# Kernel optimization log

Hardware: AMD Instinct MI355X
Metric: run time of the kernel (lower is better)

Reference implementation:

```python
import jax, jax.numpy as jnp
import numpy as np

B, N, D, L = 4, 512, 128, 2


def setup_inputs() -> dict:
    key = jax.random.key(0)
    ks = jax.random.split(key, 6)
    node_feats = jax.random.normal(ks[0], (B, N, D), dtype=jnp.float32)
    adj_mask = jax.random.uniform(ks[1], (B, N, N), dtype=jnp.float32)
    # torch Linear weights: [out_features, in_features]
    w1 = jax.random.normal(ks[2], (L, D, 2 * D), dtype=jnp.float32) * 0.05
    b1 = jax.random.normal(ks[3], (L, D), dtype=jnp.float32) * 0.05
    w2 = jax.random.normal(ks[4], (L, D, D), dtype=jnp.float32) * 0.05
    b2 = jax.random.normal(ks[5], (L, D), dtype=jnp.float32) * 0.05
    return {"node_feats": node_feats, "adj_mask": adj_mask,
            "w1": w1, "b1": b1, "w2": w2, "b2": b2}


def reference(node_feats, adj_mask, w1, b1, w2, b2):
    h = node_feats
    d = h.shape[-1]
    n_layers = w1.shape[0]
    for l in range(n_layers):
        # cat([hi, hj]) @ W1^T == hi @ Wi^T + hj @ Wj^T  (avoid 2D concat)
        wi = w1[l][:, :d]   # [D, D]
        wj = w1[l][:, d:]   # [D, D]
        ai = jnp.einsum('bnd,od->bno', h, wi)  # contribution of node i
        aj = jnp.einsum('bnd,od->bno', h, wj)  # contribution of node j
        # [B, N(i), N(j), D]
        m = jax.nn.relu(ai[:, :, None, :] + aj[:, None, :, :] + b1[l])
        m = jnp.einsum('bijd,od->bijo', m, w2[l]) + b2[l]
        m = m * adj_mask[..., None]
        msg = m.sum(axis=2)  # sum over j
        h = h + msg
    return h
```

## Files before the change

kernel.cpp:

```cpp
#include <hip/hip_runtime.h>


constexpr int Bc = 4, Nc = 512, Dc = 128, Lc = 2;
constexpr int BN = Bc * Nc;
constexpr int TIB = 4;
constexpr int TN = 4;

__global__ void transpose_w_kernel(const float* __restrict__ w1,
                                   const float* __restrict__ w2,
                                   float* __restrict__ wiT,
                                   float* __restrict__ wjT,
                                   float* __restrict__ w2T) {
    int idx = blockIdx.x * blockDim.x + threadIdx.x;
    if (idx >= Lc * Dc * Dc) return;
    int l = idx / (Dc * Dc);
    int rem = idx - l * Dc * Dc;
    int d = rem / Dc;
    int o = rem - d * Dc;
    wiT[idx] = w1[(l * Dc + o) * (2 * Dc) + d];
    wjT[idx] = w1[(l * Dc + o) * (2 * Dc) + Dc + d];
    w2T[idx] = w2[(l * Dc + o) * Dc + d];
}

__global__ __launch_bounds__(128) void gnn_lin1(const float* __restrict__ h,
                                                const float* __restrict__ wiT,
                                                const float* __restrict__ wjT,
                                                const float* __restrict__ b1,
                                                float* __restrict__ ai,
                                                float* __restrict__ aj) {
    __shared__ float hs[TN][Dc];
    const int o = threadIdx.x;
    const int r0 = blockIdx.x * TN;
#pragma unroll
    for (int t = 0; t < TN; ++t) hs[t][o] = h[(size_t)(r0 + t) * Dc + o];
    __syncthreads();
    float acci[TN], accj[TN];
    const float bo = b1[o];
#pragma unroll
    for (int t = 0; t < TN; ++t) { acci[t] = bo; accj[t] = 0.f; }
    for (int d = 0; d < Dc; d += 4) {
        float wi[4], wj[4];
#pragma unroll
        for (int k = 0; k < 4; ++k) {
            wi[k] = wiT[(size_t)(d + k) * Dc + o];
            wj[k] = wjT[(size_t)(d + k) * Dc + o];
        }
#pragma unroll
        for (int t = 0; t < TN; ++t) {
            const float4 hv = *reinterpret_cast<const float4*>(&hs[t][d]);
            acci[t] = fmaf(hv.x, wi[0], acci[t]);
            acci[t] = fmaf(hv.y, wi[1], acci[t]);
            acci[t] = fmaf(hv.z, wi[2], acci[t]);
            acci[t] = fmaf(hv.w, wi[3], acci[t]);
            accj[t] = fmaf(hv.x, wj[0], accj[t]);
            accj[t] = fmaf(hv.y, wj[1], accj[t]);
            accj[t] = fmaf(hv.z, wj[2], accj[t]);
            accj[t] = fmaf(hv.w, wj[3], accj[t]);
        }
    }
#pragma unroll
    for (int t = 0; t < TN; ++t) {
        ai[(size_t)(r0 + t) * Dc + o] = acci[t];
        aj[(size_t)(r0 + t) * Dc + o] = accj[t];
    }
}

template <bool HAS_NEXT>
__global__ __launch_bounds__(512) void gnn_msgfull(
    const float* __restrict__ ai, const float* __restrict__ aj,
    const float* __restrict__ adj, const float* __restrict__ hin,
    const float* __restrict__ w2T, const float* __restrict__ b2,
    const float* __restrict__ wiT, const float* __restrict__ wjT,
    const float* __restrict__ b1, float* __restrict__ hout,
    float* __restrict__ ai_out, float* __restrict__ aj_out) {
    __shared__ __align__(16) float adjs[TIB][Nc];
    __shared__ __align__(16) float scratch[4096];
    __shared__ float s_lds[TIB][Dc];
    __shared__ float hnew_lds[TIB][Dc];
    __shared__ float redw[8];

    const int tid = threadIdx.x;
    const int w = tid >> 6;
    const int lane = tid & 63;
    const int r0 = blockIdx.x * TIB;
    const int b = r0 >> 9;
    const int i0 = r0 & (Nc - 1);
    const float* __restrict__ ajb = aj + (size_t)b * Nc * Dc;
    const float* __restrict__ adjb = adj + (size_t)b * Nc * Nc;

    {
        const int rr = tid >> 7;
        const int c4 = (tid & 127) * 4;
        const float4 av =
            *reinterpret_cast<const float4*>(&adjb[(size_t)(i0 + rr) * Nc + c4]);
        *reinterpret_cast<float4*>(&adjs[rr][c4]) = av;
        float p = av.x + av.y + av.z + av.w;
#pragma unroll
        for (int m = 32; m >= 1; m >>= 1) p += __shfl_xor(p, m);
        if (lane == 0) redw[w] = p;
    }

    const int jlane = lane >> 5;
    const int dq = (lane & 31) * 4;
    float4 x[TIB], acc[TIB];
#pragma unroll
    for (int r = 0; r < TIB; ++r) {
        x[r] = *reinterpret_cast<const float4*>(&ai[(size_t)(r0 + r) * Dc + dq]);
        acc[r] = make_float4(0.f, 0.f, 0.f, 0.f);
    }
    __syncthreads();

    const int jw = w * 64;
    const float* __restrict__ pbase = ajb + (size_t)(jw + jlane) * Dc + dq;
#pragma unroll 4
    for (int it = 0; it < 32; ++it) {
        const float4 v = *reinterpret_cast<const float4*>(pbase + (size_t)it * 256);
        const int j = jw + 2 * it + jlane;
        const float a0 = adjs[0][j];
        const float a1 = adjs[1][j];
        const float a2 = adjs[2][j];
        const float a3 = adjs[3][j];
#define ROWF(r, a)                                                       \
        acc[r].x = fmaf(a, fmaxf(x[r].x + v.x, 0.f), acc[r].x);          \
        acc[r].y = fmaf(a, fmaxf(x[r].y + v.y, 0.f), acc[r].y);          \
        acc[r].z = fmaf(a, fmaxf(x[r].z + v.z, 0.f), acc[r].z);          \
        acc[r].w = fmaf(a, fmaxf(x[r].w + v.w, 0.f), acc[r].w);
        ROWF(0, a0) ROWF(1, a1) ROWF(2, a2) ROWF(3, a3)
#undef ROWF
    }

#pragma unroll
    for (int r = 0; r < TIB; ++r) {
        acc[r].x += __shfl_xor(acc[r].x, 32);
        acc[r].y += __shfl_xor(acc[r].y, 32);
        acc[r].z += __shfl_xor(acc[r].z, 32);
        acc[r].w += __shfl_xor(acc[r].w, 32);
    }
    if (lane < 32) {
#pragma unroll
        for (int r = 0; r < TIB; ++r)
            *reinterpret_cast<float4*>(&scratch[w * 512 + r * 128 + dq]) = acc[r];
    }
    __syncthreads();

    {
        const int rr = tid >> 7;
        const int dd = tid & 127;
        float s = 0.f;
#pragma unroll
        for (int ww = 0; ww < 8; ++ww) s += scratch[ww * 512 + rr * 128 + dd];
        s_lds[rr][dd] = s;
    }
    __syncthreads();

    {
        const int o = tid & 127;
        const int g = tid >> 7;
        float part[TIB] = {0.f, 0.f, 0.f, 0.f};
        for (int dd = g * 32; dd < g * 32 + 32; dd += 4) {
            float wv[4];
#pragma unroll
            for (int k = 0; k < 4; ++k) wv[k] = w2T[(size_t)(dd + k) * Dc + o];
#pragma unroll
            for (int r = 0; r < TIB; ++r) {
                const float4 sv = *reinterpret_cast<const float4*>(&s_lds[r][dd]);
                part[r] = fmaf(sv.x, wv[0], part[r]);
                part[r] = fmaf(sv.y, wv[1], part[r]);
                part[r] = fmaf(sv.z, wv[2], part[r]);
                part[r] = fmaf(sv.w, wv[3], part[r]);
            }
        }
#pragma unroll
        for (int r = 0; r < TIB; ++r) scratch[g * 512 + r * 128 + o] = part[r];
    }
    __syncthreads();

    {
        const int rr = tid >> 7;
        const int o = tid & 127;
        float a2c = scratch[rr * 128 + o] + scratch[512 + rr * 128 + o] +
                    scratch[1024 + rr * 128 + o] + scratch[1536 + rr * 128 + o];
        const float arow_r = redw[2 * rr] + redw[2 * rr + 1];
        const float hn =
            hin[(size_t)(r0 + rr) * Dc + o] + a2c + arow_r * b2[o];
        hout[(size_t)(r0 + rr) * Dc + o] = hn;
        if constexpr (HAS_NEXT) hnew_lds[rr][o] = hn;
    }

    if constexpr (HAS_NEXT) {
        __syncthreads();
        {
            const int o = tid & 127;
            const int g = tid >> 7;
            float pi[TIB] = {0.f, 0.f, 0.f, 0.f};
            float pj[TIB] = {0.f, 0.f, 0.f, 0.f};
            for (int dd = g * 32; dd < g * 32 + 32; dd += 4) {
                float wiv[4], wjv[4];
#pragma unroll
                for (int k = 0; k < 4; ++k) {
                    wiv[k] = wiT[(size_t)(dd + k) * Dc + o];
                    wjv[k] = wjT[(size_t)(dd + k) * Dc + o];
                }
#pragma unroll
                for (int r = 0; r < TIB; ++r) {
                    const float4 hv =
                        *reinterpret_cast<const float4*>(&hnew_lds[r][dd]);
                    pi[r] = fmaf(hv.x, wiv[0], pi[r]);
                    pi[r] = fmaf(hv.y, wiv[1], pi[r]);
                    pi[r] = fmaf(hv.z, wiv[2], pi[r]);
                    pi[r] = fmaf(hv.w, wiv[3], pi[r]);
                    pj[r] = fmaf(hv.x, wjv[0], pj[r]);
                    pj[r] = fmaf(hv.y, wjv[1], pj[r]);
                    pj[r] = fmaf(hv.z, wjv[2], pj[r]);
                    pj[r] = fmaf(hv.w, wjv[3], pj[r]);
                }
            }
#pragma unroll
            for (int r = 0; r < TIB; ++r) {
                scratch[g * 512 + r * 128 + o] = pi[r];
                scratch[2048 + g * 512 + r * 128 + o] = pj[r];
            }
        }
        __syncthreads();
        {
            const int rr = tid >> 7;
            const int o = tid & 127;
            float acci = b1[o];
            float accj = 0.f;
#pragma unroll
            for (int g = 0; g < 4; ++g) {
                acci += scratch[g * 512 + rr * 128 + o];
                accj += scratch[2048 + g * 512 + rr * 128 + o];
            }
            ai_out[(size_t)(r0 + rr) * Dc + o] = acci;
            aj_out[(size_t)(r0 + rr) * Dc + o] = accj;
        }
    }
}

extern "C" void kernel_launch(void* const* d_in, const int* in_sizes, int n_in,
                              void* d_out, int out_size, void* d_ws, size_t ws_size,
                              hipStream_t stream) {
    const float* node = (const float*)d_in[0];
    const float* adj  = (const float*)d_in[1];
    const float* w1   = (const float*)d_in[2];
    const float* b1   = (const float*)d_in[3];
    const float* w2   = (const float*)d_in[4];
    const float* b2   = (const float*)d_in[5];
    float* out = (float*)d_out;

    float* ws = (float*)d_ws;
    float* wiT = ws; ws += Lc * Dc * Dc;
    float* wjT = ws; ws += Lc * Dc * Dc;
    float* w2T = ws; ws += Lc * Dc * Dc;
    float* ai  = ws; ws += BN * Dc;
    float* aj  = ws; ws += BN * Dc;
    float* ai2 = ws; ws += BN * Dc;
    float* aj2 = ws; ws += BN * Dc;
    float* h1  = ws; ws += BN * Dc;

    transpose_w_kernel<<<(Lc * Dc * Dc + 255) / 256, 256, 0, stream>>>(
        w1, w2, wiT, wjT, w2T);

    gnn_lin1<<<BN / TN, 128, 0, stream>>>(node, wiT, wjT, b1, ai, aj);
    gnn_msgfull<true><<<BN / TIB, 512, 0, stream>>>(
        ai, aj, adj, node, w2T, b2, wiT + Dc * Dc, wjT + Dc * Dc, b1 + Dc,
        h1, ai2, aj2);
    gnn_msgfull<false><<<BN / TIB, 512, 0, stream>>>(
        ai2, aj2, adj, h1, w2T + Dc * Dc, b2 + Dc, nullptr, nullptr, nullptr,
        out, nullptr, nullptr);
}
```

Baseline: 55.02 us.

## Fuse all GNN stages into one cooperative kernel with grid syncs

Replaces the four separate launches (weight transpose, first linear, two message layers) with a single cooperative persistent kernel of 512 blocks x 256 threads that uses grid.sync between phases. Block size drops from 512 to 256 threads, and each thread covers more j and d work. The aim is to remove launch gaps and kernel-boundary overhead. The cost is grid-wide barrier latency and lower per-block parallelism, and it needs at least 2 resident blocks per CU, otherwise it falls back to the old path.

```diff
diff --git a/kernel.cpp b/kernel.cpp
--- a/kernel.cpp
+++ b/kernel.cpp
@@ -1,10 +1,239 @@
 #include <hip/hip_runtime.h>
+#include <hip/hip_cooperative_groups.h>
+
+namespace cg = cooperative_groups;
 
 
 constexpr int Bc = 4, Nc = 512, Dc = 128, Lc = 2;
 constexpr int BN = Bc * Nc;
 constexpr int TIB = 4;
 constexpr int TN = 4;
+constexpr int CTHR = 256;
+constexpr int CBLK = BN / TIB;
+
+struct SMC {
+    float adjs[TIB][Nc];
+    float scratch[4096];
+    float s_lds[TIB][Dc];
+    float hnew[TIB][Dc];
+    float redw[TIB];
+};
+
+__device__ __forceinline__ void lin1_lds_256(SMC& sm, int tid, int r0,
+                                             const float* __restrict__ wiT_l,
+                                             const float* __restrict__ wjT_l,
+                                             const float* __restrict__ b1_l,
+                                             float* __restrict__ ai_out,
+                                             float* __restrict__ aj_out) {
+    {
+        const int o = tid & 127;
+        const int g = tid >> 7;
+        float pi[TIB] = {0.f, 0.f, 0.f, 0.f};
+        float pj[TIB] = {0.f, 0.f, 0.f, 0.f};
+        for (int dd = g * 64; dd < g * 64 + 64; dd += 4) {
+            float wiv[4], wjv[4];
+#pragma unroll
+            for (int k = 0; k < 4; ++k) {
+                wiv[k] = wiT_l[(size_t)(dd + k) * Dc + o];
+                wjv[k] = wjT_l[(size_t)(dd + k) * Dc + o];
+            }
+#pragma unroll
+            for (int r = 0; r < TIB; ++r) {
+                const float4 hv = *reinterpret_cast<const float4*>(&sm.hnew[r][dd]);
+                pi[r] = fmaf(hv.x, wiv[0], pi[r]);
+                pi[r] = fmaf(hv.y, wiv[1], pi[r]);
+                pi[r] = fmaf(hv.z, wiv[2], pi[r]);
+                pi[r] = fmaf(hv.w, wiv[3], pi[r]);
+                pj[r] = fmaf(hv.x, wjv[0], pj[r]);
+                pj[r] = fmaf(hv.y, wjv[1], pj[r]);
+                pj[r] = fmaf(hv.z, wjv[2], pj[r]);
+                pj[r] = fmaf(hv.w, wjv[3], pj[r]);
+            }
+        }
+#pragma unroll
+        for (int r = 0; r < TIB; ++r) {
+            sm.scratch[g * 512 + r * 128 + o] = pi[r];
+            sm.scratch[2048 + g * 512 + r * 128 + o] = pj[r];
+        }
+    }
+    __syncthreads();
+#pragma unroll
+    for (int rep = 0; rep < 2; ++rep) {
+        const int lin = rep * 256 + tid;
+        const int rr = lin >> 7;
+        const int oo = lin & 127;
+        const float acci = b1_l[oo] + sm.scratch[rr * 128 + oo] +
+                           sm.scratch[512 + rr * 128 + oo];
+        const float accj = sm.scratch[2048 + rr * 128 + oo] +
+                           sm.scratch[2048 + 512 + rr * 128 + oo];
+        ai_out[(size_t)(r0 + rr) * Dc + oo] = acci;
+        aj_out[(size_t)(r0 + rr) * Dc + oo] = accj;
+    }
+}
+
+__device__ __forceinline__ void msg_phase_256(
+    SMC& sm, int tid, int r0, int b, int i0, const float* __restrict__ ai_in,
+    const float* __restrict__ aj_in, const float* __restrict__ adj,
+    const float* __restrict__ hin, const float* __restrict__ w2T_l,
+    const float* __restrict__ b2_l, float* __restrict__ hout, bool toLds) {
+    const int w = tid >> 6;
+    const int lane = tid & 63;
+    const float* __restrict__ ajb = aj_in + (size_t)b * Nc * Dc;
+    const float* __restrict__ adjb = adj + (size_t)b * Nc * Nc;
+
+    {
+        const int c8 = lane * 8;
+        const float4 a4 = *reinterpret_cast<const float4*>(
+            &adjb[(size_t)(i0 + w) * Nc + c8]);
+        const float4 b4 = *reinterpret_cast<const float4*>(
+            &adjb[(size_t)(i0 + w) * Nc + c8 + 4]);
+        *reinterpret_cast<float4*>(&sm.adjs[w][c8]) = a4;
+        *reinterpret_cast<float4*>(&sm.adjs[w][c8 + 4]) = b4;
+        float p = a4.x + a4.y + a4.z + a4.w + b4.x + b4.y + b4.z + b4.w;
+#pragma unroll
+        for (int m = 32; m >= 1; m >>= 1) p += __shfl_xor(p, m);
+        if (lane == 0) sm.redw[w] = p;
+    }
+
+    const int jlane = lane >> 5;
+    const int dq = (lane & 31) * 4;
+    float4 x[TIB], acc[TIB];
+#pragma unroll
+    for (int r = 0; r < TIB; ++r) {
+        x[r] = *reinterpret_cast<const float4*>(&ai_in[(size_t)(r0 + r) * Dc + dq]);
+        acc[r] = make_float4(0.f, 0.f, 0.f, 0.f);
+    }
+    __syncthreads();
+
+    const int jw = w * 128;
+    const float* __restrict__ pbase = ajb + (size_t)(jw + jlane) * Dc + dq;
+#pragma unroll 4
+    for (int it = 0; it < 64; ++it) {
+        const float4 v = *reinterpret_cast<const float4*>(pbase + (size_t)it * 256);
+        const int j = jw + 2 * it + jlane;
+        const float a0 = sm.adjs[0][j];
+        const float a1 = sm.adjs[1][j];
+        const float a2 = sm.adjs[2][j];
+        const float a3 = sm.adjs[3][j];
+#define ROWF(r, a)                                                       \
+        acc[r].x = fmaf(a, fmaxf(x[r].x + v.x, 0.f), acc[r].x);          \
+        acc[r].y = fmaf(a, fmaxf(x[r].y + v.y, 0.f), acc[r].y);          \
+        acc[r].z = fmaf(a, fmaxf(x[r].z + v.z, 0.f), acc[r].z);          \
+        acc[r].w = fmaf(a, fmaxf(x[r].w + v.w, 0.f), acc[r].w);
+        ROWF(0, a0) ROWF(1, a1) ROWF(2, a2) ROWF(3, a3)
+#undef ROWF
+    }
+
+#pragma unroll
+    for (int r = 0; r < TIB; ++r) {
+        acc[r].x += __shfl_xor(acc[r].x, 32);
+        acc[r].y += __shfl_xor(acc[r].y, 32);
+        acc[r].z += __shfl_xor(acc[r].z, 32);
+        acc[r].w += __shfl_xor(acc[r].w, 32);
+    }
+    if (lane < 32) {
+#pragma unroll
+        for (int r = 0; r < TIB; ++r)
+            *reinterpret_cast<float4*>(&sm.scratch[w * 512 + r * 128 + dq]) =
+                acc[r];
+    }
+    __syncthreads();
+
+#pragma unroll
+    for (int rep = 0; rep < 2; ++rep) {
+        const int lin = rep * 256 + tid;
+        const int rr = lin >> 7;
+        const int dd = lin & 127;
+        sm.s_lds[rr][dd] = sm.scratch[rr * 128 + dd] +
+                           sm.scratch[512 + rr * 128 + dd] +
+                           sm.scratch[1024 + rr * 128 + dd] +
+                           sm.scratch[1536 + rr * 128 + dd];
+    }
+    __syncthreads();
+
+    {
+        const int o = tid & 127;
+        const int g = tid >> 7;
+        float part[TIB] = {0.f, 0.f, 0.f, 0.f};
+        for (int dd = g * 64; dd < g * 64 + 64; dd += 4) {
+            float wv[4];
+#pragma unroll
+            for (int k = 0; k < 4; ++k) wv[k] = w2T_l[(size_t)(dd + k) * Dc + o];
+#pragma unroll
+            for (int r = 0; r < TIB; ++r) {
+                const float4 sv = *reinterpret_cast<const float4*>(&sm.s_lds[r][dd]);
+                part[r] = fmaf(sv.x, wv[0], part[r]);
+                part[r] = fmaf(sv.y, wv[1], part[r]);
+                part[r] = fmaf(sv.z, wv[2], part[r]);
+                part[r] = fmaf(sv.w, wv[3], part[r]);
+            }
+        }
+#pragma unroll
+        for (int r = 0; r < TIB; ++r) sm.scratch[g * 512 + r * 128 + o] = part[r];
+    }
+    __syncthreads();
+
+#pragma unroll
+    for (int rep = 0; rep < 2; ++rep) {
+        const int lin = rep * 256 + tid;
+        const int rr = lin >> 7;
+        const int oo = lin & 127;
+        const float a2c =
+            sm.scratch[rr * 128 + oo] + sm.scratch[512 + rr * 128 + oo];
+        const float hn = hin[(size_t)(r0 + rr) * Dc + oo] + a2c +
+                         sm.redw[rr] * b2_l[oo];
+        hout[(size_t)(r0 + rr) * Dc + oo] = hn;
+        if (toLds) sm.hnew[rr][oo] = hn;
+    }
+}
+
+__global__ __launch_bounds__(CTHR) void gnn_all(
+    const float* __restrict__ node, const float* __restrict__ adj,
+    const float* __restrict__ w1, const float* __restrict__ b1,
+    const float* __restrict__ w2, const float* __restrict__ b2,
+    float* __restrict__ out, float* __restrict__ wiT, float* __restrict__ wjT,
+    float* __restrict__ w2T, float* __restrict__ ai, float* __restrict__ aj,
+    float* __restrict__ ai2, float* __restrict__ aj2, float* __restrict__ h1) {
+    cg::grid_group grid = cg::this_grid();
+    __shared__ SMC sm;
+    const int tid = threadIdx.x;
+    const int blk = blockIdx.x;
+    const int r0 = blk * TIB;
+    const int b = r0 >> 9;
+    const int i0 = r0 & (Nc - 1);
+
+    {
+        const int idx = blk * CTHR + tid;
+        if (idx < Lc * Dc * Dc) {
+            const int l = idx >> 14;
+            const int rem = idx & (Dc * Dc - 1);
+            const int d = rem >> 7;
+            const int o = rem & 127;
+            wiT[idx] = w1[(size_t)(l * Dc + o) * (2 * Dc) + d];
+            wjT[idx] = w1[(size_t)(l * Dc + o) * (2 * Dc) + Dc + d];
+            w2T[idx] = w2[(size_t)(l * Dc + o) * Dc + d];
+        }
+    }
+    grid.sync();
+
+#pragma unroll
+    for (int rep = 0; rep < 2; ++rep) {
+        const int lin = rep * 256 + tid;
+        sm.hnew[lin >> 7][lin & 127] =
+            node[(size_t)(r0 + (lin >> 7)) * Dc + (lin & 127)];
+    }
+    __syncthreads();
+    lin1_lds_256(sm, tid, r0, wiT, wjT, b1, ai, aj);
+    grid.sync();
+
+    msg_phase_256(sm, tid, r0, b, i0, ai, aj, adj, node, w2T, b2, h1, true);
+    __syncthreads();
+    lin1_lds_256(sm, tid, r0, wiT + Dc * Dc, wjT + Dc * Dc, b1 + Dc, ai2, aj2);
+    grid.sync();
+
+    msg_phase_256(sm, tid, r0, b, i0, ai2, aj2, adj, h1, w2T + Dc * Dc, b2 + Dc,
+                  out, false);
+}
 
 __global__ void transpose_w_kernel(const float* __restrict__ w1,
                                    const float* __restrict__ w2,
@@ -181,8 +410,7 @@
         float a2c = scratch[rr * 128 + o] + scratch[512 + rr * 128 + o] +
                     scratch[1024 + rr * 128 + o] + scratch[1536 + rr * 128 + o];
         const float arow_r = redw[2 * rr] + redw[2 * rr + 1];
-        const float hn =
-            hin[(size_t)(r0 + rr) * Dc + o] + a2c + arow_r * b2[o];
+        const float hn = hin[(size_t)(r0 + rr) * Dc + o] + a2c + arow_r * b2[o];
         hout[(size_t)(r0 + rr) * Dc + o] = hn;
         if constexpr (HAS_NEXT) hnew_lds[rr][o] = hn;
     }
@@ -259,14 +487,33 @@
     float* aj2 = ws; ws += BN * Dc;
     float* h1  = ws; ws += BN * Dc;
 
-    transpose_w_kernel<<<(Lc * Dc * Dc + 255) / 256, 256, 0, stream>>>(
-        w1, w2, wiT, wjT, w2T);
-
-    gnn_lin1<<<BN / TN, 128, 0, stream>>>(node, wiT, wjT, b1, ai, aj);
-    gnn_msgfull<true><<<BN / TIB, 512, 0, stream>>>(
-        ai, aj, adj, node, w2T, b2, wiT + Dc * Dc, wjT + Dc * Dc, b1 + Dc,
-        h1, ai2, aj2);
-    gnn_msgfull<false><<<BN / TIB, 512, 0, stream>>>(
-        ai2, aj2, adj, h1, w2T + Dc * Dc, b2 + Dc, nullptr, nullptr, nullptr,
-        out, nullptr, nullptr);
-}
+    int maxBlk = 0;
+    hipError_t qe =
+        hipOccupancyMaxActiveBlocksPerMultiprocessor(&maxBlk, gnn_all, CTHR, 0);
+    bool coop = (qe == hipSuccess) && (maxBlk >= 2);
+
+    if (coop) {
+        void* kargs[] = {(void*)&node, (void*)&adj, (void*)&w1,  (void*)&b1,
+                         (void*)&w2,   (void*)&b2,  (void*)&out, (void*)&wiT,
+                         (void*)&wjT,  (void*)&w2T, (void*)&ai,  (void*)&aj,
+                         (void*)&ai2,  (void*)&aj2, (void*)&h1};
+        hipError_t le = hipLaunchCooperativeKernel(
+            (const void*)gnn_all, dim3(CBLK), dim3(CTHR), kargs, 0, stream);
+        if (le != hipSuccess) {
+            (void)hipGetLastError();
+            coop = false;
+        }
+    }
+
+    if (!coop) {
+        transpose_w_kernel<<<(Lc * Dc * Dc + 255) / 256, 256, 0, stream>>>(
+            w1, w2, wiT, wjT, w2T);
+        gnn_lin1<<<BN / TN, 128, 0, stream>>>(node, wiT, wjT, b1, ai, aj);
+        gnn_msgfull<true><<<BN / TIB, 512, 0, stream>>>(
+            ai, aj, adj, node, w2T, b2, wiT + Dc * Dc, wjT + Dc * Dc, b1 + Dc,
+            h1, ai2, aj2);
+        gnn_msgfull<false><<<BN / TIB, 512, 0, stream>>>(
+            ai2, aj2, adj, h1, w2T + Dc * Dc, b2 + Dc, nullptr, nullptr,
+            nullptr, out, nullptr, nullptr);
+    }
+}
```

Result: no change. 54.75 us (-0.5%).
